# Kernel optimization log

Hardware: AMD Instinct MI355X
Metric: run time of the kernel (lower is better)

The kernel has to match this reference:

```python
import jax, jax.numpy as jnp
import numpy as np

H = 1024      # hidden_size
NH = 16       # attention heads
DH = H // NH  # head dim
B, S = 4, 2048
EPS = 1e-12


def setup_inputs() -> dict:
    key = jax.random.key(0)
    ks = jax.random.split(key, 9)
    sc = 1.0 / np.sqrt(H)
    inp = {
        "input_tensor": jax.random.normal(ks[0], (B, S, H), dtype=jnp.float32),
        "Wq": jax.random.normal(ks[1], (H, H), dtype=jnp.float32) * sc,
        "bq": jnp.zeros((H,), jnp.float32),
        "Wk": jax.random.normal(ks[2], (H, H), dtype=jnp.float32) * sc,
        "bk": jnp.zeros((H,), jnp.float32),
        "Wv": jax.random.normal(ks[3], (H, H), dtype=jnp.float32) * sc,
        "bv": jnp.zeros((H,), jnp.float32),
        "Wo": jax.random.normal(ks[4], (H, H), dtype=jnp.float32) * sc,
        "bo": jnp.zeros((H,), jnp.float32),
        "gamma": jnp.ones((H,), jnp.float32),
        "beta": jnp.zeros((H,), jnp.float32),
    }
    return inp


def _heads(x):
    # [B,S,H] -> [B,NH,S,DH]
    b, s, _ = x.shape
    return x.reshape(b, s, NH, DH).transpose(0, 2, 1, 3)


def reference(input_tensor, Wq, bq, Wk, bk, Wv, bv, Wo, bo, gamma, beta):
    q = _heads(input_tensor @ Wq.T + bq)
    k = _heads(input_tensor @ Wk.T + bk)
    v = _heads(input_tensor @ Wv.T + bv)
    scores = jnp.einsum("bhqd,bhkd->bhqk", q, k) / jnp.sqrt(jnp.float32(DH))
    probs = jax.nn.softmax(scores, axis=-1)  # dropout p=0 -> identity
    ctx = jnp.einsum("bhqk,bhkd->bhqd", probs, v)
    ctx = ctx.transpose(0, 2, 1, 3).reshape(input_tensor.shape)  # [B,S,H]
    h = ctx @ Wo.T + bo
    x = h + input_tensor
    u = jnp.mean(x, axis=-1, keepdims=True)
    s2 = jnp.mean((x - u) ** 2, axis=-1, keepdims=True)
    xn = (x - u) / jnp.sqrt(s2 + EPS)
    return gamma * xn + beta
```

## Files before the change

kernel.cpp:

```cpp
#include <hip/hip_runtime.h>
#include <math.h>

#define H   1024
#define NH  16
#define DH  64
#define BB  4
#define SS  2048
#define M_ROWS (BB*SS)
#define EPS 1e-12f
#define QSCALE 0.18033688011112042f

typedef __attribute__((ext_vector_type(4))) float f32x4;
typedef __attribute__((ext_vector_type(8))) short bf16x8;
typedef const __attribute__((address_space(1))) void* as1cvp;
typedef __attribute__((address_space(3))) void*       as3vp;
typedef const __attribute__((address_space(1))) ushort* as1u;
typedef __attribute__((address_space(3))) ushort*       as3u;

__device__ __forceinline__ unsigned short f2bf(float f) {
    union { float f; unsigned u; } x; x.f = f;
    unsigned r = x.u + 0x7fffu + ((x.u >> 16) & 1u);
    return (unsigned short)(r >> 16);
}
__device__ __forceinline__ unsigned pk2bf(float lo, float hi) {
    return __builtin_amdgcn_perm(__float_as_uint(hi), __float_as_uint(lo), 0x07060302u);
}

__global__ __launch_bounds__(256)
void cvt_all(const float4* __restrict__ x,
             const float4* __restrict__ wq, const float4* __restrict__ wk,
             const float4* __restrict__ wv, const float4* __restrict__ wo,
             ushort4* __restrict__ xb, ushort4* __restrict__ wqb,
             ushort4* __restrict__ wkb, ushort4* __restrict__ wvb,
             ushort4* __restrict__ wob)
{
    int id = blockIdx.x * 256 + threadIdx.x;
    const float4* src; ushort4* dst; int off;
    if (id < 2097152) { src = x; dst = xb; off = id; }
    else {
        int t = id - 2097152, wsel = t >> 18;
        off = t & 262143;
        src = wsel == 0 ? wq : wsel == 1 ? wk : wsel == 2 ? wv : wo;
        dst = wsel == 0 ? wqb : wsel == 1 ? wkb : wsel == 2 ? wvb : wob;
    }
    float4 v = src[off];
    ushort4 o; o.x = f2bf(v.x); o.y = f2bf(v.y); o.z = f2bf(v.z); o.w = f2bf(v.w);
    dst[off] = o;
}

__device__ __forceinline__ void gemm_core_128(const ushort* __restrict__ A,
                                              const ushort* __restrict__ Wt,
                                              ushort* ldsP,
                                              int row0, int col0, int K,
                                              f32x4 (&acc)[4][4])
{
    const int tid = threadIdx.x, lane = tid & 63, w = tid >> 6;
    const int wr = w >> 1, wc = w & 1, l15 = lane & 15, quad = lane >> 4;
    const int lr = lane >> 2, kc = lane & 3;
    const int qs  = kc ^ ((lr >> 1) & 3);
    const int qsw = (quad ^ ((l15 >> 1) & 3)) * 8;

    const as1u gA = (as1u)A;
    const as1u gB = (as1u)Wt;
    as3u lds = (as3u)ldsP;

    const int ra = (w * 2) * 16 + lr;
    const int rb = ra + 16;
    const size_t gAr0 = (size_t)(row0 + ra) * K + qs * 8;
    const size_t gAr1 = (size_t)(row0 + rb) * K + qs * 8;
    const size_t gBr0 = (size_t)(col0 + ra) * K + qs * 8;
    const size_t gBr1 = (size_t)(col0 + rb) * K + qs * 8;
    const int dA0 = (w * 2 + 0) * 512;
    const int dA1 = (w * 2 + 1) * 512;

    __builtin_amdgcn_global_load_lds((as1cvp)(gA + gAr0), (as3vp)(lds + dA0), 16, 0, 0);
    __builtin_amdgcn_global_load_lds((as1cvp)(gA + gAr1), (as3vp)(lds + dA1), 16, 0, 0);
    __builtin_amdgcn_global_load_lds((as1cvp)(gB + gBr0), (as3vp)(lds + 4096 + dA0), 16, 0, 0);
    __builtin_amdgcn_global_load_lds((as1cvp)(gB + gBr1), (as3vp)(lds + 4096 + dA1), 16, 0, 0);

    int bofs = 0;
    for (int k0 = 0; k0 < K; k0 += 32) {
        __syncthreads();
        const int nofs = bofs ^ 8192;
        if (k0 + 32 < K) {
            __builtin_amdgcn_global_load_lds((as1cvp)(gA + gAr0 + k0 + 32),
                                             (as3vp)(lds + nofs + dA0), 16, 0, 0);
            __builtin_amdgcn_global_load_lds((as1cvp)(gA + gAr1 + k0 + 32),
                                             (as3vp)(lds + nofs + dA1), 16, 0, 0);
            __builtin_amdgcn_global_load_lds((as1cvp)(gB + gBr0 + k0 + 32),
                                             (as3vp)(lds + nofs + 4096 + dA0), 16, 0, 0);
            __builtin_amdgcn_global_load_lds((as1cvp)(gB + gBr1 + k0 + 32),
                                             (as3vp)(lds + nofs + 4096 + dA1), 16, 0, 0);
        }
        const ushort* AsP = ldsP + bofs;
        const ushort* BsP = ldsP + bofs + 4096;
        bf16x8 af[4], bfr[4];
        #pragma unroll
        for (int rt = 0; rt < 4; ++rt)
            af[rt] = *(const bf16x8*)&AsP[(wr * 64 + rt * 16 + l15) * 32 + qsw];
        #pragma unroll
        for (int ct = 0; ct < 4; ++ct)
            bfr[ct] = *(const bf16x8*)&BsP[(wc * 64 + ct * 16 + l15) * 32 + qsw];
        #pragma unroll
        for (int rt = 0; rt < 4; ++rt)
            #pragma unroll
            for (int ct = 0; ct < 4; ++ct)
                acc[rt][ct] = __builtin_amdgcn_mfma_f32_16x16x32_bf16(af[rt], bfr[ct], acc[rt][ct], 0, 0, 0);
        bofs = nofs;
    }
}

__global__ __launch_bounds__(256, 3)
void qkv_gemm(const ushort* __restrict__ xb,
              const ushort* __restrict__ Wqb, const ushort* __restrict__ Wkb,
              const ushort* __restrict__ Wvb,
              const float* __restrict__ bq, const float* __restrict__ bk,
              const float* __restrict__ bv,
              ushort* __restrict__ Qb, ushort* __restrict__ Kb, ushort* __restrict__ Vt)
{
    __shared__ __align__(16) ushort Ls[4 * 4096];
    const int lin = blockIdx.x;
    const int swz = (lin & 7) * 192 + (lin >> 3);
    const int z   = swz >> 9;
    const int rem = swz & 511;
    const int row0 = (rem >> 3) * 128;
    const int col0 = (rem & 7) * 128;

    const ushort* Wt  = z == 0 ? Wqb : z == 1 ? Wkb : Wvb;
    const float* bias = z == 0 ? bq  : z == 1 ? bk  : bv;

    f32x4 acc[4][4];
    #pragma unroll
    for (int i = 0; i < 4; ++i)
        #pragma unroll
        for (int j = 0; j < 4; ++j)
            acc[i][j] = (f32x4){0.f, 0.f, 0.f, 0.f};

    gemm_core_128(xb, Wt, Ls, row0, col0, H, acc);

    const int tid = threadIdx.x, lane = tid & 63, w = tid >> 6;
    const int wr = w >> 1, wc = w & 1, l15 = lane & 15, quad = lane >> 4;

    #pragma unroll
    for (int rt = 0; rt < 4; ++rt) {
        const int r0g = row0 + wr * 64 + rt * 16 + quad * 4;
        #pragma unroll
        for (int ct = 0; ct < 4; ++ct) {
            const int c = col0 + wc * 64 + ct * 16 + l15;
            const float bs = bias[c];
            if (z == 0) {
                #pragma unroll
                for (int i = 0; i < 4; ++i)
                    Qb[(size_t)(r0g + i) * H + c] = f2bf((acc[rt][ct][i] + bs) * QSCALE);
            } else if (z == 1) {
                #pragma unroll
                for (int i = 0; i < 4; ++i)
                    Kb[(size_t)(r0g + i) * H + c] = f2bf(acc[rt][ct][i] + bs);
            } else {
                const int bb = r0g >> 11, s0 = r0g & 2047;
                const int hh = c >> 6, dd = c & 63;
                ushort4 o;
                o.x = f2bf(acc[rt][ct][0] + bs);
                o.y = f2bf(acc[rt][ct][1] + bs);
                o.z = f2bf(acc[rt][ct][2] + bs);
                o.w = f2bf(acc[rt][ct][3] + bs);
                *(ushort4*)&Vt[(((size_t)(bb * 16 + hh) * 64 + dd) << 11) + s0] = o;
            }
        }
    }
}

__global__ __launch_bounds__(256, 3)
void oproj_gemm(const ushort* __restrict__ ctxb, const ushort* __restrict__ Wob,
                const float* __restrict__ bo, const float* __restrict__ res,
                float* __restrict__ Xr)
{
    __shared__ __align__(16) ushort Ls[4 * 4096];
    const int lin = blockIdx.x;
    const int swz = (lin & 7) * 64 + (lin >> 3);
    const int row0 = (swz >> 3) * 128;
    const int col0 = (swz & 7) * 128;

    f32x4 acc[4][4];
    #pragma unroll
    for (int i = 0; i < 4; ++i)
        #pragma unroll
        for (int j = 0; j < 4; ++j)
            acc[i][j] = (f32x4){0.f, 0.f, 0.f, 0.f};

    gemm_core_128(ctxb, Wob, Ls, row0, col0, H, acc);

    const int tid = threadIdx.x, lane = tid & 63, w = tid >> 6;
    const int wr = w >> 1, wc = w & 1, l15 = lane & 15, quad = lane >> 4;

    #pragma unroll
    for (int rt = 0; rt < 4; ++rt) {
        const int r0g = row0 + wr * 64 + rt * 16 + quad * 4;
        #pragma unroll
        for (int ct = 0; ct < 4; ++ct) {
            const int c = col0 + wc * 64 + ct * 16 + l15;
            const float bs = bo[c];
            #pragma unroll
            for (int i = 0; i < 4; ++i) {
                size_t idx = (size_t)(r0g + i) * H + c;
                Xr[idx] = acc[rt][ct][i] + bs + res[idx];
            }
        }
    }
}

#define KTILE 64
#define NKT (SS / KTILE)

__global__ __launch_bounds__(256, 3)
void flash_attn_mfma(const ushort* __restrict__ Qb, const ushort* __restrict__ Kb,
                     const ushort* __restrict__ Vt, ushort* __restrict__ ctx)
{
    __shared__ __align__(16) ushort Ks[2][KTILE * 64];
    __shared__ __align__(16) ushort Vs[2][64 * KTILE];

    const int tid  = threadIdx.x;
    const int lane = tid & 63;
    const int w    = tid >> 6;
    const int l15  = lane & 15, quad = lane >> 4;
    const int bh   = blockIdx.x & 63;
    const int qt   = blockIdx.x >> 6;
    const int b    = bh >> 4, h = bh & 15;
    const int row0 = qt * 128 + w * 32;
    const size_t qk_base = (size_t)(b * SS) * H + h * DH;
    const size_t vt_base = (size_t)((b * 16 + h) * 64) * SS;

    const as1u gK = (const as1u)Kb;
    const as1u gV = (const as1u)Vt;

    const int srow = lane >> 3;
    const int c8   = lane & 7;
    const int sck0 = c8 ^ ((srow & 3) | (((w * 2 + 0) & 1) << 2));
    const int sck1 = c8 ^ ((srow & 3) | (((w * 2 + 1) & 1) << 2));

    const int fL = (l15 & 3) | (((l15 >> 2) & 1) << 2);
    const int fV = (l15 & 3) | (((l15 >> 3) & 1) << 2);
    const int rA = 8 * (l15 >> 2) + (l15 & 3);
    int kOff0[4], kOff1[4], vOff0[4], vOff1[4];
    #pragma unroll
    for (int ct = 0; ct < 4; ++ct) {
        const int r = rA + (ct & 1) * 4 + (ct >> 1) * 32;
        kOff0[ct] = r * 64 + ((quad ^ fL) * 8);
        kOff1[ct] = r * 64 + (((4 | quad) ^ fL) * 8);
    }
    #pragma unroll
    for (int dt = 0; dt < 4; ++dt) {
        const int rv = dt * 16 + l15;
        vOff0[dt] = rv * 64 + ((quad ^ fV) * 8);
        vOff1[dt] = rv * 64 + (((4 | quad) ^ fV) * 8);
    }

    bf16x8 aq[2][2];
    #pragma unroll
    for (int g = 0; g < 2; ++g) {
        const size_t qrow = qk_base + (size_t)(row0 + g * 16 + l15) * H;
        aq[g][0] = *(const bf16x8*)&Qb[qrow + quad * 8];
        aq[g][1] = *(const bf16x8*)&Qb[qrow + 32 + quad * 8];
    }

    union { unsigned u[4]; bf16x8 v; } ONES;
    #pragma unroll
    for (int i = 0; i < 4; ++i) ONES.u[i] = 0x3F803F80u;

    f32x4 acc_l[2];
    f32x4 o[2][4];
    #pragma unroll
    for (int g = 0; g < 2; ++g) {
        acc_l[g] = (f32x4){0.f, 0.f, 0.f, 0.f};
        #pragma unroll
        for (int dt = 0; dt < 4; ++dt) o[g][dt] = (f32x4){0.f, 0.f, 0.f, 0.f};
    }

    const as1u gK0 = gK + qk_base + (size_t)(w * 16 + srow) * H;
    const as1u gV0 = gV + vt_base + (size_t)(w * 16 + srow) * SS;

    __builtin_amdgcn_global_load_lds((as1cvp)(gK0 + sck0 * 8),
                                     (as3vp)(&Ks[0][(w * 16) * 64]), 16, 0, 0);
    __builtin_amdgcn_global_load_lds((as1cvp)(gK0 + (size_t)8 * H + sck1 * 8),
                                     (as3vp)(&Ks[0][(w * 16 + 8) * 64]), 16, 0, 0);
    __builtin_amdgcn_global_load_lds((as1cvp)(gV0 + sck0 * 8),
                                     (as3vp)(&Vs[0][(w * 16) * 64]), 16, 0, 0);
    __builtin_amdgcn_global_load_lds((as1cvp)(gV0 + (size_t)8 * SS + sck1 * 8),
                                     (as3vp)(&Vs[0][(w * 16 + 8) * 64]), 16, 0, 0);

    for (int kt = 0; kt < NKT; ++kt) {
        __syncthreads();

        if (kt + 1 < NKT) {
            const int j0 = (kt + 1) * KTILE;
            const int nb = (kt + 1) & 1;
            __builtin_amdgcn_global_load_lds((as1cvp)(gK0 + (size_t)j0 * H + sck0 * 8),
                                             (as3vp)(&Ks[nb][(w * 16) * 64]), 16, 0, 0);
            __builtin_amdgcn_global_load_lds((as1cvp)(gK0 + (size_t)(j0 + 8) * H + sck1 * 8),
                                             (as3vp)(&Ks[nb][(w * 16 + 8) * 64]), 16, 0, 0);
            __builtin_amdgcn_global_load_lds((as1cvp)(gV0 + j0 + sck0 * 8),
                                             (as3vp)(&Vs[nb][(w * 16) * 64]), 16, 0, 0);
            __builtin_amdgcn_global_load_lds((as1cvp)(gV0 + (size_t)8 * SS + j0 + sck1 * 8),
                                             (as3vp)(&Vs[nb][(w * 16 + 8) * 64]), 16, 0, 0);
        }

        const ushort* Ktile = Ks[kt & 1];
        const ushort* Vtile = Vs[kt & 1];

        f32x4 s[2][4];
        __builtin_amdgcn_s_setprio(1);
        #pragma unroll
        for (int ct = 0; ct < 4; ++ct) {
            const bf16x8 k0 = *(const bf16x8*)&Ktile[kOff0[ct]];
            const bf16x8 k1 = *(const bf16x8*)&Ktile[kOff1[ct]];
            #pragma unroll
            for (int g = 0; g < 2; ++g) {
                f32x4 z = (f32x4){0.f, 0.f, 0.f, 0.f};
                z = __builtin_amdgcn_mfma_f32_16x16x32_bf16(k0, aq[g][0], z, 0, 0, 0);
                z = __builtin_amdgcn_mfma_f32_16x16x32_bf16(k1, aq[g][1], z, 0, 0, 0);
                s[g][ct] = z;
            }
        }
        __builtin_amdgcn_s_setprio(0);

        union { unsigned u[4]; bf16x8 v; } A[2][2];
        #pragma unroll
        for (int g = 0; g < 2; ++g) {
            #pragma unroll
            for (int ct = 0; ct < 4; ++ct) {
                const float p0 = __builtin_amdgcn_exp2f(s[g][ct][0]);
                const float p1 = __builtin_amdgcn_exp2f(s[g][ct][1]);
                const float p2 = __builtin_amdgcn_exp2f(s[g][ct][2]);
                const float p3 = __builtin_amdgcn_exp2f(s[g][ct][3]);
                A[g][ct >> 1].u[(ct & 1) * 2 + 0] = pk2bf(p0, p1);
                A[g][ct >> 1].u[(ct & 1) * 2 + 1] = pk2bf(p2, p3);
            }
        }

        __builtin_amdgcn_s_setprio(1);
        #pragma unroll
        for (int g = 0; g < 2; ++g) {
            acc_l[g] = __builtin_amdgcn_mfma_f32_16x16x32_bf16(A[g][0].v, ONES.v, acc_l[g], 0, 0, 0);
            acc_l[g] = __builtin_amdgcn_mfma_f32_16x16x32_bf16(A[g][1].v, ONES.v, acc_l[g], 0, 0, 0);
        }
        #pragma unroll
        for (int dt = 0; dt < 4; ++dt) {
            const bf16x8 v0 = *(const bf16x8*)&Vtile[vOff0[dt]];
            const bf16x8 v1 = *(const bf16x8*)&Vtile[vOff1[dt]];
            #pragma unroll
            for (int g = 0; g < 2; ++g) {
                o[g][dt] = __builtin_amdgcn_mfma_f32_16x16x32_bf16(A[g][0].v, v0, o[g][dt], 0, 0, 0);
                o[g][dt] = __builtin_amdgcn_mfma_f32_16x16x32_bf16(A[g][1].v, v1, o[g][dt], 0, 0, 0);
            }
        }
        __builtin_amdgcn_s_setprio(0);
    }

    #pragma unroll
    for (int g = 0; g < 2; ++g) {
        #pragma unroll
        for (int i = 0; i < 4; ++i) {
            const float inv = 1.f / acc_l[g][i];
            const int r = row0 + g * 16 + quad * 4 + i;
            #pragma unroll
            for (int dt = 0; dt < 4; ++dt)
                ctx[qk_base + (size_t)r * H + dt * 16 + l15] = f2bf(o[g][dt][i] * inv);
        }
    }
}

__global__ __launch_bounds__(256)
void ln_kernel(const float* __restrict__ Xr, const float* __restrict__ gamma,
               const float* __restrict__ beta, float* __restrict__ out)
{
    __shared__ float red[4], red2[4];
    const int row = blockIdx.x;
    const int tid = threadIdx.x;
    const int lane = tid & 63, w = tid >> 6;
    const float4 v = ((const float4*)(Xr + (size_t)row * H))[tid];
    float s  = v.x + v.y + v.z + v.w;
    float ss = v.x * v.x + v.y * v.y + v.z * v.z + v.w * v.w;
    #pragma unroll
    for (int d = 1; d < 64; d <<= 1) {
        s  += __shfl_xor(s, d);
        ss += __shfl_xor(ss, d);
    }
    if (lane == 0) { red[w] = s; red2[w] = ss; }
    __syncthreads();
    s  = red[0]  + red[1]  + red[2]  + red[3];
    ss = red2[0] + red2[1] + red2[2] + red2[3];
    const float mean = s * (1.f / H);
    const float var  = ss * (1.f / H) - mean * mean;
    const float rstd = rsqrtf(var + EPS);
    const float4 g  = ((const float4*)gamma)[tid];
    const float4 be = ((const float4*)beta)[tid];
    float4 o;
    o.x = g.x * (v.x - mean) * rstd + be.x;
    o.y = g.y * (v.y - mean) * rstd + be.y;
    o.z = g.z * (v.z - mean) * rstd + be.z;
    o.w = g.w * (v.w - mean) * rstd + be.w;
    ((float4*)(out + (size_t)row * H))[tid] = o;
}

extern "C" void kernel_launch(void* const* d_in, const int* in_sizes, int n_in,
                              void* d_out, int out_size, void* d_ws, size_t ws_size,
                              hipStream_t stream)
{
    const float* x     = (const float*)d_in[0];
    const float* Wq    = (const float*)d_in[1];
    const float* bq    = (const float*)d_in[2];
    const float* Wk    = (const float*)d_in[3];
    const float* bk    = (const float*)d_in[4];
    const float* Wv    = (const float*)d_in[5];
    const float* bv    = (const float*)d_in[6];
    const float* Wo    = (const float*)d_in[7];
    const float* bo    = (const float*)d_in[8];
    const float* gamma = (const float*)d_in[9];
    const float* beta  = (const float*)d_in[10];

    char* ws = (char*)d_ws;
    ushort* xb  = (ushort*)(ws);
    ushort* Wqb = (ushort*)(ws + (size_t)(16 << 20));
    ushort* Wkb = (ushort*)(ws + (size_t)(18 << 20));
    ushort* Wvb = (ushort*)(ws + (size_t)(20 << 20));
    ushort* Wob = (ushort*)(ws + (size_t)(22 << 20));
    ushort* Qb  = (ushort*)(ws + (size_t)(24 << 20));
    ushort* Kb  = (ushort*)(ws + (size_t)(40 << 20));
    ushort* Vt  = (ushort*)(ws + (size_t)(56 << 20));
    float*  Xr  = (float*) (ws + (size_t)(40 << 20));

    cvt_all<<<12288, 256, 0, stream>>>((const float4*)x, (const float4*)Wq, (const float4*)Wk,
                                       (const float4*)Wv, (const float4*)Wo,
                                       (ushort4*)xb, (ushort4*)Wqb, (ushort4*)Wkb,
                                       (ushort4*)Wvb, (ushort4*)Wob);

    qkv_gemm<<<1536, 256, 0, stream>>>(
        xb, Wqb, Wkb, Wvb, bq, bk, bv, Qb, Kb, Vt);

    flash_attn_mfma<<<BB * NH * (SS / 128), 256, 0, stream>>>(Qb, Kb, Vt, Qb );

    oproj_gemm<<<512, 256, 0, stream>>>(Qb, Wob, bo, x, Xr);

    ln_kernel<<<M_ROWS, 256, 0, stream>>>(Xr, gamma, beta, (float*)d_out);
}
```

Before: 281.5 us.

## Triple-buffer GEMM LDS pipeline and double attention rows per wave

The shared GEMM core moves from a double-buffered LDS pipeline with a full syncthreads each step to a three-stage ring. It prefetches two K-steps ahead and waits with explicit vmcnt counters before a raw barrier, aiming to hide global-to-LDS latency. Separately, the flash attention kernel now gives each wave 64 query rows instead of 32, so each K/V tile loaded into LDS is reused across twice as many rows, and it launches half as many blocks. This raises register pressure, so launch bounds drop to 2 blocks per CU, and the smaller grid of 512 blocks may underfill the GPU.

```diff
diff --git a/kernel.cpp b/kernel.cpp
--- a/kernel.cpp
+++ b/kernel.cpp
@@ -48,6 +48,16 @@
     dst[off] = o;
 }
 
+#define STAGE_QKV(ofs, k0)                                                              \
+    __builtin_amdgcn_global_load_lds((as1cvp)(gA + gAr0 + (k0)),                        \
+                                     (as3vp)(lds + (ofs) + dA0), 16, 0, 0);             \
+    __builtin_amdgcn_global_load_lds((as1cvp)(gA + gAr1 + (k0)),                        \
+                                     (as3vp)(lds + (ofs) + dA1), 16, 0, 0);             \
+    __builtin_amdgcn_global_load_lds((as1cvp)(gB + gBr0 + (k0)),                        \
+                                     (as3vp)(lds + (ofs) + 4096 + dA0), 16, 0, 0);      \
+    __builtin_amdgcn_global_load_lds((as1cvp)(gB + gBr1 + (k0)),                        \
+                                     (as3vp)(lds + (ofs) + 4096 + dA1), 16, 0, 0);
+
 __device__ __forceinline__ void gemm_core_128(const ushort* __restrict__ A,
                                               const ushort* __restrict__ Wt,
                                               ushort* ldsP,
@@ -73,27 +83,20 @@
     const int dA0 = (w * 2 + 0) * 512;
     const int dA1 = (w * 2 + 1) * 512;
 
-    __builtin_amdgcn_global_load_lds((as1cvp)(gA + gAr0), (as3vp)(lds + dA0), 16, 0, 0);
-    __builtin_amdgcn_global_load_lds((as1cvp)(gA + gAr1), (as3vp)(lds + dA1), 16, 0, 0);
-    __builtin_amdgcn_global_load_lds((as1cvp)(gB + gBr0), (as3vp)(lds + 4096 + dA0), 16, 0, 0);
-    __builtin_amdgcn_global_load_lds((as1cvp)(gB + gBr1), (as3vp)(lds + 4096 + dA1), 16, 0, 0);
-
-    int bofs = 0;
+    STAGE_QKV(0, 0);
+    STAGE_QKV(8192, 32);
+
+    int cur = 0;
     for (int k0 = 0; k0 < K; k0 += 32) {
-        __syncthreads();
-        const int nofs = bofs ^ 8192;
-        if (k0 + 32 < K) {
-            __builtin_amdgcn_global_load_lds((as1cvp)(gA + gAr0 + k0 + 32),
-                                             (as3vp)(lds + nofs + dA0), 16, 0, 0);
-            __builtin_amdgcn_global_load_lds((as1cvp)(gA + gAr1 + k0 + 32),
-                                             (as3vp)(lds + nofs + dA1), 16, 0, 0);
-            __builtin_amdgcn_global_load_lds((as1cvp)(gB + gBr0 + k0 + 32),
-                                             (as3vp)(lds + nofs + 4096 + dA0), 16, 0, 0);
-            __builtin_amdgcn_global_load_lds((as1cvp)(gB + gBr1 + k0 + 32),
-                                             (as3vp)(lds + nofs + 4096 + dA1), 16, 0, 0);
-        }
-        const ushort* AsP = ldsP + bofs;
-        const ushort* BsP = ldsP + bofs + 4096;
+        if (k0 + 32 < K) asm volatile("s_waitcnt vmcnt(4)" ::: "memory");
+        else             asm volatile("s_waitcnt vmcnt(0)" ::: "memory");
+        __builtin_amdgcn_s_barrier();
+
+        int nxt2 = cur + 16384; if (nxt2 >= 24576) nxt2 -= 24576;
+        if (k0 + 64 < K) { STAGE_QKV(nxt2, k0 + 64); }
+
+        const ushort* AsP = ldsP + cur;
+        const ushort* BsP = ldsP + cur + 4096;
         bf16x8 af[4], bfr[4];
         #pragma unroll
         for (int rt = 0; rt < 4; ++rt)
@@ -106,7 +109,8 @@
             #pragma unroll
             for (int ct = 0; ct < 4; ++ct)
                 acc[rt][ct] = __builtin_amdgcn_mfma_f32_16x16x32_bf16(af[rt], bfr[ct], acc[rt][ct], 0, 0, 0);
-        bofs = nofs;
+
+        cur += 8192; if (cur == 24576) cur = 0;
     }
 }
 
@@ -118,7 +122,7 @@
               const float* __restrict__ bv,
               ushort* __restrict__ Qb, ushort* __restrict__ Kb, ushort* __restrict__ Vt)
 {
-    __shared__ __align__(16) ushort Ls[4 * 4096];
+    __shared__ __align__(16) ushort Ls[3 * 8192];
     const int lin = blockIdx.x;
     const int swz = (lin & 7) * 192 + (lin >> 3);
     const int z   = swz >> 9;
@@ -175,7 +179,7 @@
                 const float* __restrict__ bo, const float* __restrict__ res,
                 float* __restrict__ Xr)
 {
-    __shared__ __align__(16) ushort Ls[4 * 4096];
+    __shared__ __align__(16) ushort Ls[3 * 8192];
     const int lin = blockIdx.x;
     const int swz = (lin & 7) * 64 + (lin >> 3);
     const int row0 = (swz >> 3) * 128;
@@ -212,7 +216,7 @@
 #define KTILE 64
 #define NKT (SS / KTILE)
 
-__global__ __launch_bounds__(256, 3)
+__global__ __launch_bounds__(256, 2)
 void flash_attn_mfma(const ushort* __restrict__ Qb, const ushort* __restrict__ Kb,
                      const ushort* __restrict__ Vt, ushort* __restrict__ ctx)
 {
@@ -226,7 +230,7 @@
     const int bh   = blockIdx.x & 63;
     const int qt   = blockIdx.x >> 6;
     const int b    = bh >> 4, h = bh & 15;
-    const int row0 = qt * 128 + w * 32;
+    const int row0 = qt * 256 + w * 64;
     const size_t qk_base = (size_t)(b * SS) * H + h * DH;
     const size_t vt_base = (size_t)((b * 16 + h) * 64) * SS;
 
@@ -255,9 +259,9 @@
         vOff1[dt] = rv * 64 + (((4 | quad) ^ fV) * 8);
     }
 
-    bf16x8 aq[2][2];
-    #pragma unroll
-    for (int g = 0; g < 2; ++g) {
+    bf16x8 aq[4][2];
+    #pragma unroll
+    for (int g = 0; g < 4; ++g) {
         const size_t qrow = qk_base + (size_t)(row0 + g * 16 + l15) * H;
         aq[g][0] = *(const bf16x8*)&Qb[qrow + quad * 8];
         aq[g][1] = *(const bf16x8*)&Qb[qrow + 32 + quad * 8];
@@ -267,10 +271,10 @@
     #pragma unroll
     for (int i = 0; i < 4; ++i) ONES.u[i] = 0x3F803F80u;
 
-    f32x4 acc_l[2];
-    f32x4 o[2][4];
-    #pragma unroll
-    for (int g = 0; g < 2; ++g) {
+    f32x4 acc_l[4];
+    f32x4 o[4][4];
+    #pragma unroll
+    for (int g = 0; g < 4; ++g) {
         acc_l[g] = (f32x4){0.f, 0.f, 0.f, 0.f};
         #pragma unroll
         for (int dt = 0; dt < 4; ++dt) o[g][dt] = (f32x4){0.f, 0.f, 0.f, 0.f};
@@ -307,14 +311,14 @@
         const ushort* Ktile = Ks[kt & 1];
         const ushort* Vtile = Vs[kt & 1];
 
-        f32x4 s[2][4];
+        f32x4 s[4][4];
         __builtin_amdgcn_s_setprio(1);
         #pragma unroll
         for (int ct = 0; ct < 4; ++ct) {
             const bf16x8 k0 = *(const bf16x8*)&Ktile[kOff0[ct]];
             const bf16x8 k1 = *(const bf16x8*)&Ktile[kOff1[ct]];
             #pragma unroll
-            for (int g = 0; g < 2; ++g) {
+            for (int g = 0; g < 4; ++g) {
                 f32x4 z = (f32x4){0.f, 0.f, 0.f, 0.f};
                 z = __builtin_amdgcn_mfma_f32_16x16x32_bf16(k0, aq[g][0], z, 0, 0, 0);
                 z = __builtin_amdgcn_mfma_f32_16x16x32_bf16(k1, aq[g][1], z, 0, 0, 0);
@@ -323,9 +327,9 @@
         }
         __builtin_amdgcn_s_setprio(0);
 
-        union { unsigned u[4]; bf16x8 v; } A[2][2];
-        #pragma unroll
-        for (int g = 0; g < 2; ++g) {
+        union { unsigned u[4]; bf16x8 v; } A[4][2];
+        #pragma unroll
+        for (int g = 0; g < 4; ++g) {
             #pragma unroll
             for (int ct = 0; ct < 4; ++ct) {
                 const float p0 = __builtin_amdgcn_exp2f(s[g][ct][0]);
@@ -339,7 +343,7 @@
 
         __builtin_amdgcn_s_setprio(1);
         #pragma unroll
-        for (int g = 0; g < 2; ++g) {
+        for (int g = 0; g < 4; ++g) {
             acc_l[g] = __builtin_amdgcn_mfma_f32_16x16x32_bf16(A[g][0].v, ONES.v, acc_l[g], 0, 0, 0);
             acc_l[g] = __builtin_amdgcn_mfma_f32_16x16x32_bf16(A[g][1].v, ONES.v, acc_l[g], 0, 0, 0);
         }
@@ -348,7 +352,7 @@
             const bf16x8 v0 = *(const bf16x8*)&Vtile[vOff0[dt]];
             const bf16x8 v1 = *(const bf16x8*)&Vtile[vOff1[dt]];
             #pragma unroll
-            for (int g = 0; g < 2; ++g) {
+            for (int g = 0; g < 4; ++g) {
                 o[g][dt] = __builtin_amdgcn_mfma_f32_16x16x32_bf16(A[g][0].v, v0, o[g][dt], 0, 0, 0);
                 o[g][dt] = __builtin_amdgcn_mfma_f32_16x16x32_bf16(A[g][1].v, v1, o[g][dt], 0, 0, 0);
             }
@@ -357,7 +361,7 @@
     }
 
     #pragma unroll
-    for (int g = 0; g < 2; ++g) {
+    for (int g = 0; g < 4; ++g) {
         #pragma unroll
         for (int i = 0; i < 4; ++i) {
             const float inv = 1.f / acc_l[g][i];
@@ -437,7 +441,7 @@
     qkv_gemm<<<1536, 256, 0, stream>>>(
         xb, Wqb, Wkb, Wvb, bq, bk, bv, Qb, Kb, Vt);
 
-    flash_attn_mfma<<<BB * NH * (SS / 128), 256, 0, stream>>>(Qb, Kb, Vt, Qb );
+    flash_attn_mfma<<<BB * NH * (SS / 256), 256, 0, stream>>>(Qb, Kb, Vt, Qb );
 
     oproj_gemm<<<512, 256, 0, stream>>>(Qb, Wob, bo, x, Xr);
 
```

After: 275.1 us. 1.02x faster.
